# Kernel optimization log

Hardware: AMD Instinct MI355X
Metric: run time of the kernel (lower is better)

Reference implementation:

```python
import jax, jax.numpy as jnp
import numpy as np

N = 50000      # n_nodes
E = 400000     # edges per snapshot
T = 7          # end_day - start_day + 1
S = T + 1      # snapshots needed (incl. adjs[end_day+1])
NHID = 128     # nhid_gcn
NOUT = 64      # gcn output / gru input
NGRU = 64      # gru hidden
NHN = 64       # nhid_nodes
BN_EPS = 1e-5


def _unif(k, shape, fan):
    s = 1.0 / np.sqrt(fan)
    return jax.random.uniform(k, shape, jnp.float32, -s, s)


def setup_inputs() -> dict:
    key = jax.random.key(0)
    ks = jax.random.split(key, 16)
    adj_idx = jax.random.randint(ks[0], (S, 2, E), 0, N, dtype=jnp.int32)
    adj_val = jax.random.uniform(ks[1], (S, E), dtype=jnp.float32)
    return {
        'adj_idx': adj_idx, 'adj_val': adj_val,
        'start_day': 0, 'end_day': 6,
        # GCN layers (uniform(-1/sqrt(out), 1/sqrt(out)) like reset_parameters)
        'W1': _unif(ks[2], (N, NHID), NHID), 'b1': _unif(ks[3], (NHID,), NHID),
        'W2': _unif(ks[4], (NHID, NOUT), NOUT), 'b2': _unif(ks[5], (NOUT,), NOUT),
        # GRU (torch layout: [3*H, in] / [3*H, H], gate order r,z,n)
        'w_ih': _unif(ks[6], (3 * NGRU, NOUT), NGRU), 'w_hh': _unif(ks[7], (3 * NGRU, NGRU), NGRU),
        'b_ih': _unif(ks[8], (3 * NGRU,), NGRU), 'b_hh': _unif(ks[9], (3 * NGRU,), NGRU),
        'bn_gamma': jnp.ones((NGRU,), jnp.float32), 'bn_beta': jnp.zeros((NGRU,), jnp.float32),
        'attn_w': _unif(ks[10], (2 * NGRU, 1), 2 * NGRU), 'attn_b': _unif(ks[11], (1,), 2 * NGRU),
        'np_w1': _unif(ks[12], (2 * NGRU, NHN), 2 * NGRU), 'np_b1': _unif(ks[13], (NHN,), 2 * NGRU),
        'np_w2': _unif(ks[14], (NHN, 2), NHN), 'np_b2': _unif(ks[15], (2,), NHN),
    }


def _spmm(row, col, val, x):
    # sparse.mm(adj, x): out[r] = sum_{(r,c)} val * x[c]
    return jax.ops.segment_sum(val[:, None] * x[col], row, num_segments=N)


def _forward(adj_idx, start_day, end_day, adj_val, W1, b1, W2, b2,
             w_ih, w_hh, b_ih, b_hh, bn_gamma, bn_beta,
             attn_w, attn_b, np_w1, np_b1, np_w2, np_b2):
    seq_idx = adj_idx[start_day:end_day + 1]   # [T,2,E]
    seq_val = adj_val[start_day:end_day + 1]   # [T,E]

    def step(h, ts):
        idx, val = ts
        row, col = idx[0], idx[1]
        # GCN layer 1: feat is identity => support == W1
        x = jax.nn.relu(_spmm(row, col, val, W1) + b1)           # [N,NHID]
        # GCN layer 2 (no activation on last layer)
        x = _spmm(row, col, val, x @ W2) + b2                    # [N,NOUT]
        # GRU cell (batch = nodes)
        gi = x @ w_ih.T + b_ih
        gh = h @ w_hh.T + b_hh
        ir, iz, in_ = jnp.split(gi, 3, axis=1)
        hr, hz, hn = jnp.split(gh, 3, axis=1)
        r = jax.nn.sigmoid(ir + hr)
        z = jax.nn.sigmoid(iz + hz)
        n = jnp.tanh(in_ + r * hn)
        return (1.0 - z) * n + z * h, None

    h0 = jnp.zeros((N, NGRU), adj_val.dtype)
    final_emb, _ = jax.lax.scan(step, h0, (seq_idx, seq_val))    # [N,NGRU]

    # BatchNorm1d (training-mode batch stats, biased variance)
    mean = final_emb.mean(axis=0)
    var = final_emb.var(axis=0)
    final_emb = (final_emb - mean) / jnp.sqrt(var + BN_EPS) * bn_gamma + bn_beta

    # get_node_an_scores on adjs[end_day+1]
    idx = adj_idx[end_day + 1]
    row, col = idx[0], idx[1]
    mask = row != col                                            # drop self loops
    deg = jax.ops.segment_sum(mask.astype(final_emb.dtype), row, num_segments=N)
    inv_deg = jnp.where(deg != 0, 1.0 / jnp.maximum(deg, 1.0), 1.0)
    nbr = final_emb[col]                                         # [E,NGRU]
    weights = jax.nn.sigmoid(
        jnp.concatenate([final_emb[row], nbr], axis=1) @ attn_w + attn_b)  # [E,1]
    ev = jnp.where(mask, inv_deg[row] * weights[:, 0], 0.0)
    neigh = jax.ops.segment_sum(ev[:, None] * nbr, row, num_segments=N)    # [N,NGRU]
    z = jnp.concatenate([final_emb, neigh], axis=1)
    h1 = jax.nn.relu(z @ np_w1 + np_b1)
    pred = jax.nn.log_softmax(h1 @ np_w2 + np_b2, axis=1)        # [N,2]
    return pred


def reference(adj_idx, adj_val, start_day, end_day, W1, b1, W2, b2,
              w_ih, w_hh, b_ih, b_hh, bn_gamma, bn_beta,
              attn_w, attn_b, np_w1, np_b1, np_w2, np_b2):
    return _forward(adj_idx, start_day, end_day, adj_val, W1, b1, W2, b2,
                    w_ih, w_hh, b_ih, b_hh, bn_gamma, bn_beta,
                    attn_w, attn_b, np_w1, np_b1, np_w2, np_b2)
```

## Files before the change

### kernel.cpp

```cpp
#include <hip/hip_runtime.h>
#include <math.h>

#define N_NODES 50000
#define N_EDGES 400000
#define NHID 128
#define NOUT 64
#define NGRU 64
#define BN_EPS 1e-5f
#define T_STEPS 7
#define FINAL_DAY 7
#define NPAD 50176
#define NBLK 196

__device__ __forceinline__ float sigmoidf_(float x) { return 1.f / (1.f + expf(-x)); }

__global__ void hist_kernel(const int* __restrict__ row, int* __restrict__ cnt) {
    int e = blockIdx.x * blockDim.x + threadIdx.x;
    if (e < N_EDGES) atomicAdd(&cnt[row[e]], 1);
}

__global__ void scan1_kernel(const int* __restrict__ cnt, int* __restrict__ off,
                             int* __restrict__ bsum) {
    __shared__ int s[256];
    int tid = threadIdx.x;
    int gid = blockIdx.x * 256 + tid;
    int v = cnt[gid];
    s[tid] = v;
    __syncthreads();
    for (int d = 1; d < 256; d <<= 1) {
        int t = (tid >= d) ? s[tid - d] : 0;
        __syncthreads();
        s[tid] += t;
        __syncthreads();
    }
    off[gid] = s[tid];
    if (tid == 255) bsum[blockIdx.x] = s[255];
}

__global__ void scan2_kernel(int* __restrict__ bsum) {
    __shared__ int s[256];
    int tid = threadIdx.x;
    s[tid] = (tid < NBLK) ? bsum[tid] : 0;
    __syncthreads();
    for (int d = 1; d < 256; d <<= 1) {
        int t = (tid >= d) ? s[tid - d] : 0;
        __syncthreads();
        s[tid] += t;
        __syncthreads();
    }
    if (tid < NBLK) bsum[tid] = s[tid];
}

__global__ void scan3_kernel(const int* __restrict__ cnt, int* __restrict__ off,
                             const int* __restrict__ bsum, int* __restrict__ wcur) {
    int gid = blockIdx.x * 256 + threadIdx.x;
    if (gid < N_NODES) {
        int ex = off[gid] - cnt[gid] + (blockIdx.x ? bsum[blockIdx.x - 1] : 0);
        off[gid] = ex;
        wcur[gid] = ex;
    }
    if (gid == 0) off[N_NODES] = N_EDGES;
}

__global__ void scatter_kernel(const int* __restrict__ row, const int* __restrict__ col,
                               const float* __restrict__ val, int* __restrict__ wcur,
                               int* __restrict__ colp, float* __restrict__ valp) {
    int e = blockIdx.x * blockDim.x + threadIdx.x;
    if (e >= N_EDGES) return;
    int r = row[e];
    int p = atomicAdd(&wcur[r], 1);
    colp[p] = col[e];
    valp[p] = val[e];
}

__global__ __launch_bounds__(256) void fused_gcn_gather(
    const int* __restrict__ off, const int* __restrict__ colp,
    const float* __restrict__ valp, const float* __restrict__ W1,
    const float* __restrict__ b1, const float* __restrict__ W2,
    float* __restrict__ y) {
    int lane = threadIdx.x & 63;
    float wcol[NHID];
#pragma unroll
    for (int k = 0; k < NHID; ++k) wcol[k] = W2[(size_t)k * NOUT + lane];
    float b1a = b1[lane * 2], b1b = b1[lane * 2 + 1];
    int wave = (blockIdx.x * blockDim.x + threadIdx.x) >> 6;
    int nwaves = (gridDim.x * blockDim.x) >> 6;
    for (int n = wave; n < N_NODES; n += nwaves) {
        int beg = off[n], end = off[n + 1];
        float accx = 0.f, accy = 0.f;
        for (int base = beg; base < end; base += 64) {
            int m = end - base; if (m > 64) m = 64;
            int ce = 0; float ve = 0.f;
            if (lane < m) { ce = colp[base + lane]; ve = valp[base + lane]; }
#pragma unroll 4
            for (int k = 0; k < m; ++k) {
                int c = __shfl(ce, k);
                float v = __shfl(ve, k);
                const float2 w = *reinterpret_cast<const float2*>(W1 + (size_t)c * NHID + lane * 2);
                accx += v * w.x; accy += v * w.y;
            }
        }
        float xa = fmaxf(accx + b1a, 0.f);
        float xb = fmaxf(accy + b1b, 0.f);
        float acc = 0.f;
#pragma unroll
        for (int k2 = 0; k2 < 64; ++k2) {
            float x0 = __shfl(xa, k2);
            float x1v = __shfl(xb, k2);
            acc += x0 * wcol[2 * k2] + x1v * wcol[2 * k2 + 1];
        }
        y[(size_t)n * NOUT + lane] = acc;
    }
}

__global__ __launch_bounds__(256) void spmm2_gather(
    const int* __restrict__ off, const int* __restrict__ colp,
    const float* __restrict__ valp, const float* __restrict__ y,
    float* __restrict__ x2) {
    int lane = threadIdx.x & 63;
    int wave = (blockIdx.x * blockDim.x + threadIdx.x) >> 6;
    int nwaves = (gridDim.x * blockDim.x) >> 6;
    for (int n = wave; n < N_NODES; n += nwaves) {
        int beg = off[n], end = off[n + 1];
        float acc = 0.f;
        for (int base = beg; base < end; base += 64) {
            int m = end - base; if (m > 64) m = 64;
            int ce = 0; float ve = 0.f;
            if (lane < m) { ce = colp[base + lane]; ve = valp[base + lane]; }
#pragma unroll 4
            for (int k = 0; k < m; ++k) {
                int c = __shfl(ce, k);
                float v = __shfl(ve, k);
                acc += v * y[(size_t)c * NOUT + lane];
            }
        }
        x2[(size_t)n * NOUT + lane] = acc;
    }
}

__global__ void bias_fold(const float* __restrict__ w_ih, const float* __restrict__ b2,
                          const float* __restrict__ b_ih, float* __restrict__ bias_i) {
    int f = blockIdx.x * 64 + threadIdx.x;
    if (f >= 192) return;
    float acc = b_ih[f];
    for (int k = 0; k < 64; ++k) acc += w_ih[(size_t)f * 64 + k] * b2[k];
    bias_i[f] = acc;
}

__global__ __launch_bounds__(256) void gru_gemm(const float* __restrict__ x2,
                                                const float* __restrict__ w_ih,
                                                const float* __restrict__ w_hh,
                                                const float* __restrict__ bias_i,
                                                const float* __restrict__ b_hh,
                                                float* __restrict__ h) {
    __shared__ float XT[64 * 64];
    __shared__ float WT[64 * 192];
    int tid = threadIdx.x;
    int n0 = blockIdx.x * 64;
    int tf = tid & 15, tn = tid >> 4;

    float gi[4][12], gh[4][12];
#pragma unroll
    for (int i = 0; i < 4; ++i)
#pragma unroll
        for (int j = 0; j < 12; ++j) { gi[i][j] = 0.f; gh[i][j] = 0.f; }

#pragma unroll
    for (int r = 0; r < 4; ++r) {
        int idx = r * 256 + tid;
        int n = idx & 63, c4 = idx >> 6;
        int node = n0 + n;
        float4 v = make_float4(0.f, 0.f, 0.f, 0.f);
        if (node < N_NODES) v = *reinterpret_cast<const float4*>(x2 + (size_t)node * 64 + c4 * 4);
        XT[(c4 * 4 + 0) * 64 + n] = v.x;
        XT[(c4 * 4 + 1) * 64 + n] = v.y;
        XT[(c4 * 4 + 2) * 64 + n] = v.z;
        XT[(c4 * 4 + 3) * 64 + n] = v.w;
    }
#pragma unroll
    for (int r = 0; r < 12; ++r) {
        int idx = r * 256 + tid;
        int f = idx % 192, c4 = idx / 192;
        float4 v = *reinterpret_cast<const float4*>(w_ih + (size_t)f * 64 + c4 * 4);
        WT[(c4 * 4 + 0) * 192 + f] = v.x;
        WT[(c4 * 4 + 1) * 192 + f] = v.y;
        WT[(c4 * 4 + 2) * 192 + f] = v.z;
        WT[(c4 * 4 + 3) * 192 + f] = v.w;
    }
    __syncthreads();

#pragma unroll 4
    for (int k = 0; k < 64; ++k) {
        float4 a  = *reinterpret_cast<const float4*>(XT + k * 64 + tn * 4);
        float4 br = *reinterpret_cast<const float4*>(WT + k * 192 + tf * 4);
        float4 bz = *reinterpret_cast<const float4*>(WT + k * 192 + 64 + tf * 4);
        float4 bn = *reinterpret_cast<const float4*>(WT + k * 192 + 128 + tf * 4);
        float av[4] = {a.x, a.y, a.z, a.w};
#pragma unroll
        for (int i = 0; i < 4; ++i) {
            gi[i][0] += av[i] * br.x; gi[i][1] += av[i] * br.y;
            gi[i][2] += av[i] * br.z; gi[i][3] += av[i] * br.w;
            gi[i][4] += av[i] * bz.x; gi[i][5] += av[i] * bz.y;
            gi[i][6] += av[i] * bz.z; gi[i][7] += av[i] * bz.w;
            gi[i][8] += av[i] * bn.x; gi[i][9] += av[i] * bn.y;
            gi[i][10] += av[i] * bn.z; gi[i][11] += av[i] * bn.w;
        }
    }
    __syncthreads();

#pragma unroll
    for (int r = 0; r < 4; ++r) {
        int idx = r * 256 + tid;
        int n = idx & 63, c4 = idx >> 6;
        int node = n0 + n;
        float4 v = make_float4(0.f, 0.f, 0.f, 0.f);
        if (node < N_NODES) v = *reinterpret_cast<const float4*>(h + (size_t)node * 64 + c4 * 4);
        XT[(c4 * 4 + 0) * 64 + n] = v.x;
        XT[(c4 * 4 + 1) * 64 + n] = v.y;
        XT[(c4 * 4 + 2) * 64 + n] = v.z;
        XT[(c4 * 4 + 3) * 64 + n] = v.w;
    }
#pragma unroll
    for (int r = 0; r < 12; ++r) {
        int idx = r * 256 + tid;
        int f = idx % 192, c4 = idx / 192;
        float4 v = *reinterpret_cast<const float4*>(w_hh + (size_t)f * 64 + c4 * 4);
        WT[(c4 * 4 + 0) * 192 + f] = v.x;
        WT[(c4 * 4 + 1) * 192 + f] = v.y;
        WT[(c4 * 4 + 2) * 192 + f] = v.z;
        WT[(c4 * 4 + 3) * 192 + f] = v.w;
    }
    __syncthreads();

#pragma unroll 4
    for (int k = 0; k < 64; ++k) {
        float4 a  = *reinterpret_cast<const float4*>(XT + k * 64 + tn * 4);
        float4 br = *reinterpret_cast<const float4*>(WT + k * 192 + tf * 4);
        float4 bz = *reinterpret_cast<const float4*>(WT + k * 192 + 64 + tf * 4);
        float4 bn = *reinterpret_cast<const float4*>(WT + k * 192 + 128 + tf * 4);
        float av[4] = {a.x, a.y, a.z, a.w};
#pragma unroll
        for (int i = 0; i < 4; ++i) {
            gh[i][0] += av[i] * br.x; gh[i][1] += av[i] * br.y;
            gh[i][2] += av[i] * br.z; gh[i][3] += av[i] * br.w;
            gh[i][4] += av[i] * bz.x; gh[i][5] += av[i] * bz.y;
            gh[i][6] += av[i] * bz.z; gh[i][7] += av[i] * bz.w;
            gh[i][8] += av[i] * bn.x; gh[i][9] += av[i] * bn.y;
            gh[i][10] += av[i] * bn.z; gh[i][11] += av[i] * bn.w;
        }
    }

    int f0 = tf * 4;
    float bir[4], biz[4], bin_[4], bhr[4], bhz[4], bhn[4];
#pragma unroll
    for (int j = 0; j < 4; ++j) {
        bir[j] = bias_i[f0 + j];
        biz[j] = bias_i[64 + f0 + j];
        bin_[j] = bias_i[128 + f0 + j];
        bhr[j] = b_hh[f0 + j];
        bhz[j] = b_hh[64 + f0 + j];
        bhn[j] = b_hh[128 + f0 + j];
    }
#pragma unroll
    for (int i = 0; i < 4; ++i) {
        int node = n0 + tn * 4 + i;
        float hnew[4];
#pragma unroll
        for (int j = 0; j < 4; ++j) {
            float r = sigmoidf_(gi[i][j] + bir[j] + gh[i][j] + bhr[j]);
            float z = sigmoidf_(gi[i][4 + j] + biz[j] + gh[i][4 + j] + bhz[j]);
            float nn = tanhf(gi[i][8 + j] + bin_[j] + r * (gh[i][8 + j] + bhn[j]));
            float hold = XT[(f0 + j) * 64 + tn * 4 + i];
            hnew[j] = (1.f - z) * nn + z * hold;
        }
        if (node < N_NODES) {
            float4 v = make_float4(hnew[0], hnew[1], hnew[2], hnew[3]);
            *reinterpret_cast<float4*>(h + (size_t)node * 64 + f0) = v;
        }
    }
}

__global__ void bn_stats(const float* __restrict__ h, float* __restrict__ bnsum,
                         float* __restrict__ bnsq) {
    int gid = blockIdx.x * blockDim.x + threadIdx.x;
    int wave = gid >> 6, lane = gid & 63;
    int nw = (gridDim.x * blockDim.x) >> 6;
    float s = 0.f, sq = 0.f;
    for (int n = wave; n < N_NODES; n += nw) {
        float v = h[(size_t)n * NGRU + lane];
        s += v; sq += v * v;
    }
    atomicAdd(&bnsum[lane], s);
    atomicAdd(&bnsq[lane], sq);
}

__global__ void bn_norm(float* __restrict__ h, const float* __restrict__ bnsum,
                        const float* __restrict__ bnsq, const float* __restrict__ gamma,
                        const float* __restrict__ beta) {
    int gid = blockIdx.x * blockDim.x + threadIdx.x;
    if (gid >= N_NODES * NGRU) return;
    int f = gid & 63;
    float mean = bnsum[f] * (1.f / N_NODES);
    float var = bnsq[f] * (1.f / N_NODES) - mean * mean;
    float scale = gamma[f] * rsqrtf(var + BN_EPS);
    h[gid] = (h[gid] - mean) * scale + beta[f];
}

__global__ __launch_bounds__(256) void attn_gather(
    const int* __restrict__ off, const int* __restrict__ colp,
    const float* __restrict__ emb, const float* __restrict__ attn_w,
    const float* __restrict__ attn_b, float* __restrict__ neigh) {
    int lane = threadIdx.x & 63;
    float aw1 = attn_w[lane], aw2 = attn_w[64 + lane];
    float ab0 = attn_b[0];
    int wave = (blockIdx.x * blockDim.x + threadIdx.x) >> 6;
    int nwaves = (gridDim.x * blockDim.x) >> 6;
    for (int r = wave; r < N_NODES; r += nwaves) {
        float er = emb[(size_t)r * NGRU + lane];
        float pr = er * aw1;
#pragma unroll
        for (int o = 32; o > 0; o >>= 1) pr += __shfl_xor(pr, o);
        int beg = off[r], end = off[r + 1];
        float acc = 0.f;
        int cntv = 0;
        for (int base = beg; base < end; base += 64) {
            int m = end - base; if (m > 64) m = 64;
            int ce = 0;
            if (lane < m) ce = colp[base + lane];
            for (int k = 0; k < m; ++k) {
                int c = __shfl(ce, k);
                if (c == r) continue;
                float ec = emb[(size_t)c * NGRU + lane];
                float pe = ec * aw2;
#pragma unroll
                for (int o = 32; o > 0; o >>= 1) pe += __shfl_xor(pe, o);
                float wgt = sigmoidf_(pr + pe + ab0);
                acc += wgt * ec;
                ++cntv;
            }
        }
        float d = (float)cntv;
        float inv = (d != 0.f) ? 1.f / fmaxf(d, 1.f) : 1.f;
        neigh[(size_t)r * NGRU + lane] = acc * inv;
    }
}

__global__ __launch_bounds__(256) void pred_kernel(const float* __restrict__ emb,
                                                   const float* __restrict__ neigh,
                                                   const float* __restrict__ np_w1,
                                                   const float* __restrict__ np_b1,
                                                   const float* __restrict__ np_w2,
                                                   const float* __restrict__ np_b2,
                                                   float* __restrict__ out) {
    int lane = threadIdx.x & 63;
    float wcol[128];
#pragma unroll
    for (int k = 0; k < 128; ++k) wcol[k] = np_w1[(size_t)k * 64 + lane];
    float b1l = np_b1[lane];
    float w20 = np_w2[lane * 2], w21 = np_w2[lane * 2 + 1];
    float b20 = np_b2[0], b21 = np_b2[1];
    int wave = (blockIdx.x * blockDim.x + threadIdx.x) >> 6;
    int nwaves = (gridDim.x * blockDim.x) >> 6;
    for (int n = wave; n < N_NODES; n += nwaves) {
        float ev = emb[(size_t)n * 64 + lane];
        float nv = neigh[(size_t)n * 64 + lane];
        float acc = b1l;
#pragma unroll
        for (int k2 = 0; k2 < 64; ++k2) {
            float e = __shfl(ev, k2);
            float nn = __shfl(nv, k2);
            acc += e * wcol[k2] + nn * wcol[64 + k2];
        }
        float h1 = fmaxf(acc, 0.f);
        float l0 = h1 * w20, l1 = h1 * w21;
#pragma unroll
        for (int o = 32; o > 0; o >>= 1) {
            l0 += __shfl_xor(l0, o);
            l1 += __shfl_xor(l1, o);
        }
        if (lane == 0) {
            l0 += b20; l1 += b21;
            float m = fmaxf(l0, l1);
            float ls = m + logf(expf(l0 - m) + expf(l1 - m));
            out[(size_t)n * 2 + 0] = l0 - ls;
            out[(size_t)n * 2 + 1] = l1 - ls;
        }
    }
}

extern "C" void kernel_launch(void* const* d_in, const int* in_sizes, int n_in,
                              void* d_out, int out_size, void* d_ws, size_t ws_size,
                              hipStream_t stream) {
    const int* adj_idx = (const int*)d_in[0];
    const float* adj_val = (const float*)d_in[1];
    const float* W1 = (const float*)d_in[4];
    const float* b1 = (const float*)d_in[5];
    const float* W2 = (const float*)d_in[6];
    const float* b2 = (const float*)d_in[7];
    const float* w_ih = (const float*)d_in[8];
    const float* w_hh = (const float*)d_in[9];
    const float* b_ih = (const float*)d_in[10];
    const float* b_hh = (const float*)d_in[11];
    const float* bn_gamma = (const float*)d_in[12];
    const float* bn_beta = (const float*)d_in[13];
    const float* attn_w = (const float*)d_in[14];
    const float* attn_b = (const float*)d_in[15];
    const float* np_w1 = (const float*)d_in[16];
    const float* np_b1 = (const float*)d_in[17];
    const float* np_w2 = (const float*)d_in[18];
    const float* np_b2 = (const float*)d_in[19];
    float* out = (float*)d_out;

    float* ws = (float*)d_ws;
    float* y = ws;
    float* x2 = ws + (size_t)N_NODES * 64;
    float* h = ws + (size_t)N_NODES * 128;
    size_t p = (size_t)N_NODES * 192;
    int* off = (int*)(ws + p);    p += NPAD + 1;
    int* wcur = (int*)(ws + p);   p += N_NODES;
    int* cnt = (int*)(ws + p);    p += NPAD;
    int* bsum = (int*)(ws + p);   p += 256;
    int* colp = (int*)(ws + p);   p += N_EDGES;
    float* valp = ws + p;         p += N_EDGES;
    float* bnsum = ws + p;        p += 64;
    float* bnsq = ws + p;         p += 64;
    float* bias_i = ws + p;       p += 192;
    float* neigh = y;

    hipMemsetAsync(h, 0, (size_t)N_NODES * 64 * sizeof(float), stream);
    bias_fold<<<3, 64, 0, stream>>>(w_ih, b2, b_ih, bias_i);

    const int egrid = (N_EDGES + 255) / 256;
    const int gtiles = (N_NODES + 63) / 64;

    for (int t = 0; t < T_STEPS; ++t) {
        const int* row = adj_idx + (size_t)t * 2 * N_EDGES;
        const int* colr = row + N_EDGES;
        const float* val = adj_val + (size_t)t * N_EDGES;
        hipMemsetAsync(cnt, 0, NPAD * sizeof(int), stream);
        hist_kernel<<<egrid, 256, 0, stream>>>(row, cnt);
        scan1_kernel<<<NBLK, 256, 0, stream>>>(cnt, off, bsum);
        scan2_kernel<<<1, 256, 0, stream>>>(bsum);
        scan3_kernel<<<NBLK, 256, 0, stream>>>(cnt, off, bsum, wcur);
        scatter_kernel<<<egrid, 256, 0, stream>>>(row, colr, val, wcur, colp, valp);
        fused_gcn_gather<<<512, 256, 0, stream>>>(off, colp, valp, W1, b1, W2, y);
        spmm2_gather<<<512, 256, 0, stream>>>(off, colp, valp, y, x2);
        gru_gemm<<<gtiles, 256, 0, stream>>>(x2, w_ih, w_hh, bias_i, b_hh, h);
    }

    hipMemsetAsync(bnsum, 0, 2 * 64 * sizeof(float), stream);
    bn_stats<<<256, 256, 0, stream>>>(h, bnsum, bnsq);
    bn_norm<<<(N_NODES * 64 + 255) / 256, 256, 0, stream>>>(h, bnsum, bnsq, bn_gamma, bn_beta);

    const int* row7 = adj_idx + (size_t)FINAL_DAY * 2 * N_EDGES;
    const int* col7 = row7 + N_EDGES;
    hipMemsetAsync(cnt, 0, NPAD * sizeof(int), stream);
    hist_kernel<<<egrid, 256, 0, stream>>>(row7, cnt);
    scan1_kernel<<<NBLK, 256, 0, stream>>>(cnt, off, bsum);
    scan2_kernel<<<1, 256, 0, stream>>>(bsum);
    scan3_kernel<<<NBLK, 256, 0, stream>>>(cnt, off, bsum, wcur);
    scatter_kernel<<<egrid, 256, 0, stream>>>(row7, col7, adj_val + (size_t)FINAL_DAY * N_EDGES, wcur, colp, valp);
    attn_gather<<<512, 256, 0, stream>>>(off, colp, h, attn_w, attn_b, neigh);
    pred_kernel<<<512, 256, 0, stream>>>(h, neigh, np_w1, np_b1, np_w2, np_b2, out);
}
```

Measured before the change: 2.699 ms.

## Batch CSR builds across days, stage W2 in LDS, precompute attention projections

Builds the row histograms and prefix-scan offsets for all eight snapshots in one set of batched launches instead of five launches per day. This cuts launch count and serialization. The GCN kernel now keeps W2 in shared memory instead of 128 per-lane registers, which should relieve register pressure and raise occupancy at the cost of LDS reads in the inner loop. The attention stage precomputes the per-node neighbor projection once and computes the sigmoid weights per edge in parallel, replacing a 64-lane reduction for every edge.

```diff
diff --git a/kernel.cpp b/kernel.cpp
--- a/kernel.cpp
+++ b/kernel.cpp
@@ -9,22 +9,28 @@
 #define BN_EPS 1e-5f
 #define T_STEPS 7
 #define FINAL_DAY 7
+#define NDAYS 8
 #define NPAD 50176
 #define NBLK 196
+#define OFFS (NPAD + 1)
 
 __device__ __forceinline__ float sigmoidf_(float x) { return 1.f / (1.f + expf(-x)); }
 
-__global__ void hist_kernel(const int* __restrict__ row, int* __restrict__ cnt) {
-    int e = blockIdx.x * blockDim.x + threadIdx.x;
-    if (e < N_EDGES) atomicAdd(&cnt[row[e]], 1);
-}
-
-__global__ void scan1_kernel(const int* __restrict__ cnt, int* __restrict__ off,
-                             int* __restrict__ bsum) {
+__global__ void hist8_kernel(const int* __restrict__ adj_idx, int* __restrict__ cnt8) {
+    int g = blockIdx.x * blockDim.x + threadIdx.x;
+    if (g >= NDAYS * N_EDGES) return;
+    int day = g / N_EDGES, idx = g - day * N_EDGES;
+    int r = adj_idx[(size_t)day * 2 * N_EDGES + idx];
+    atomicAdd(&cnt8[day * NPAD + r], 1);
+}
+
+__global__ void scan1_8(const int* __restrict__ cnt8, int* __restrict__ off8,
+                        int* __restrict__ bsum8) {
     __shared__ int s[256];
+    int day = blockIdx.x / NBLK, blk = blockIdx.x - day * NBLK;
     int tid = threadIdx.x;
-    int gid = blockIdx.x * 256 + tid;
-    int v = cnt[gid];
+    int gid = blk * 256 + tid;
+    int v = cnt8[day * NPAD + gid];
     s[tid] = v;
     __syncthreads();
     for (int d = 1; d < 256; d <<= 1) {
@@ -33,14 +39,15 @@
         s[tid] += t;
         __syncthreads();
     }
-    off[gid] = s[tid];
-    if (tid == 255) bsum[blockIdx.x] = s[255];
-}
-
-__global__ void scan2_kernel(int* __restrict__ bsum) {
+    off8[day * OFFS + gid] = s[tid];
+    if (tid == 255) bsum8[day * NBLK + blk] = s[255];
+}
+
+__global__ void scan2_8(int* __restrict__ bsum8) {
     __shared__ int s[256];
+    int day = blockIdx.x;
     int tid = threadIdx.x;
-    s[tid] = (tid < NBLK) ? bsum[tid] : 0;
+    s[tid] = (tid < NBLK) ? bsum8[day * NBLK + tid] : 0;
     __syncthreads();
     for (int d = 1; d < 256; d <<= 1) {
         int t = (tid >= d) ? s[tid - d] : 0;
@@ -48,18 +55,20 @@
         s[tid] += t;
         __syncthreads();
     }
-    if (tid < NBLK) bsum[tid] = s[tid];
-}
-
-__global__ void scan3_kernel(const int* __restrict__ cnt, int* __restrict__ off,
-                             const int* __restrict__ bsum, int* __restrict__ wcur) {
-    int gid = blockIdx.x * 256 + threadIdx.x;
+    if (tid < NBLK) bsum8[day * NBLK + tid] = s[tid];
+}
+
+__global__ void scan3_8(const int* __restrict__ cnt8, int* __restrict__ off8,
+                        const int* __restrict__ bsum8, int* __restrict__ wcur8) {
+    int day = blockIdx.x / NBLK, blk = blockIdx.x - day * NBLK;
+    int gid = blk * 256 + threadIdx.x;
     if (gid < N_NODES) {
-        int ex = off[gid] - cnt[gid] + (blockIdx.x ? bsum[blockIdx.x - 1] : 0);
-        off[gid] = ex;
-        wcur[gid] = ex;
-    }
-    if (gid == 0) off[N_NODES] = N_EDGES;
+        int ex = off8[day * OFFS + gid] - cnt8[day * NPAD + gid]
+               + (blk ? bsum8[day * NBLK + blk - 1] : 0);
+        off8[day * OFFS + gid] = ex;
+        wcur8[day * N_NODES + gid] = ex;
+    }
+    if (gid == 0) off8[day * OFFS + N_NODES] = N_EDGES;
 }
 
 __global__ void scatter_kernel(const int* __restrict__ row, const int* __restrict__ col,
@@ -78,10 +87,14 @@
     const float* __restrict__ valp, const float* __restrict__ W1,
     const float* __restrict__ b1, const float* __restrict__ W2,
     float* __restrict__ y) {
+    __shared__ float W2s[NHID * NOUT];
+    {
+        const float4* src = reinterpret_cast<const float4*>(W2);
+        float4* dst = reinterpret_cast<float4*>(W2s);
+        for (int i = threadIdx.x; i < NHID * NOUT / 4; i += 256) dst[i] = src[i];
+    }
+    __syncthreads();
     int lane = threadIdx.x & 63;
-    float wcol[NHID];
-#pragma unroll
-    for (int k = 0; k < NHID; ++k) wcol[k] = W2[(size_t)k * NOUT + lane];
     float b1a = b1[lane * 2], b1b = b1[lane * 2 + 1];
     int wave = (blockIdx.x * blockDim.x + threadIdx.x) >> 6;
     int nwaves = (gridDim.x * blockDim.x) >> 6;
@@ -107,7 +120,7 @@
         for (int k2 = 0; k2 < 64; ++k2) {
             float x0 = __shfl(xa, k2);
             float x1v = __shfl(xb, k2);
-            acc += x0 * wcol[2 * k2] + x1v * wcol[2 * k2 + 1];
+            acc += x0 * W2s[(2 * k2) * 64 + lane] + x1v * W2s[(2 * k2 + 1) * 64 + lane];
         }
         y[(size_t)n * NOUT + lane] = acc;
     }
@@ -306,12 +319,28 @@
     h[gid] = (h[gid] - mean) * scale + beta[f];
 }
 
+__global__ __launch_bounds__(256) void attn_pre(const float* __restrict__ emb,
+                                                const float* __restrict__ attn_w,
+                                                float* __restrict__ pe) {
+    int lane = threadIdx.x & 63;
+    float aw2 = attn_w[64 + lane];
+    int wave = (blockIdx.x * blockDim.x + threadIdx.x) >> 6;
+    int nwaves = (gridDim.x * blockDim.x) >> 6;
+    for (int n = wave; n < N_NODES; n += nwaves) {
+        float p = emb[(size_t)n * NGRU + lane] * aw2;
+#pragma unroll
+        for (int o = 32; o > 0; o >>= 1) p += __shfl_xor(p, o);
+        if (lane == 0) pe[n] = p;
+    }
+}
+
 __global__ __launch_bounds__(256) void attn_gather(
     const int* __restrict__ off, const int* __restrict__ colp,
     const float* __restrict__ emb, const float* __restrict__ attn_w,
-    const float* __restrict__ attn_b, float* __restrict__ neigh) {
+    const float* __restrict__ attn_b, const float* __restrict__ pe,
+    float* __restrict__ neigh) {
     int lane = threadIdx.x & 63;
-    float aw1 = attn_w[lane], aw2 = attn_w[64 + lane];
+    float aw1 = attn_w[lane];
     float ab0 = attn_b[0];
     int wave = (blockIdx.x * blockDim.x + threadIdx.x) >> 6;
     int nwaves = (gridDim.x * blockDim.x) >> 6;
@@ -322,25 +351,24 @@
         for (int o = 32; o > 0; o >>= 1) pr += __shfl_xor(pr, o);
         int beg = off[r], end = off[r + 1];
         float acc = 0.f;
-        int cntv = 0;
+        float fcnt = 0.f;
         for (int base = beg; base < end; base += 64) {
             int m = end - base; if (m > 64) m = 64;
-            int ce = 0;
-            if (lane < m) ce = colp[base + lane];
+            int ce = 0; float pc = 0.f;
+            if (lane < m) { ce = colp[base + lane]; pc = pe[ce]; }
+            bool valid = (lane < m) && (ce != r);
+            float wl = valid ? sigmoidf_(pr + pc + ab0) : 0.f;
+            fcnt += valid ? 1.f : 0.f;
             for (int k = 0; k < m; ++k) {
                 int c = __shfl(ce, k);
                 if (c == r) continue;
-                float ec = emb[(size_t)c * NGRU + lane];
-                float pe = ec * aw2;
-#pragma unroll
-                for (int o = 32; o > 0; o >>= 1) pe += __shfl_xor(pe, o);
-                float wgt = sigmoidf_(pr + pe + ab0);
-                acc += wgt * ec;
-                ++cntv;
+                float w = __shfl(wl, k);
+                acc += w * emb[(size_t)c * NGRU + lane];
             }
         }
-        float d = (float)cntv;
-        float inv = (d != 0.f) ? 1.f / fmaxf(d, 1.f) : 1.f;
+#pragma unroll
+        for (int o = 32; o > 0; o >>= 1) fcnt += __shfl_xor(fcnt, o);
+        float inv = (fcnt != 0.f) ? 1.f / fmaxf(fcnt, 1.f) : 1.f;
         neigh[(size_t)r * NGRU + lane] = acc * inv;
     }
 }
@@ -416,19 +444,26 @@
     float* x2 = ws + (size_t)N_NODES * 64;
     float* h = ws + (size_t)N_NODES * 128;
     size_t p = (size_t)N_NODES * 192;
-    int* off = (int*)(ws + p);    p += NPAD + 1;
-    int* wcur = (int*)(ws + p);   p += N_NODES;
-    int* cnt = (int*)(ws + p);    p += NPAD;
-    int* bsum = (int*)(ws + p);   p += 256;
+    int* off8 = (int*)(ws + p);   p += (size_t)NDAYS * OFFS;
+    int* wcur8 = (int*)(ws + p);  p += (size_t)NDAYS * N_NODES;
+    int* cnt8 = (int*)(ws + p);   p += (size_t)NDAYS * NPAD;
+    int* bsum8 = (int*)(ws + p);  p += 2048;
     int* colp = (int*)(ws + p);   p += N_EDGES;
     float* valp = ws + p;         p += N_EDGES;
     float* bnsum = ws + p;        p += 64;
     float* bnsq = ws + p;         p += 64;
     float* bias_i = ws + p;       p += 192;
+    float* pe = ws + p;           p += N_NODES;
     float* neigh = y;
 
     hipMemsetAsync(h, 0, (size_t)N_NODES * 64 * sizeof(float), stream);
+    hipMemsetAsync(cnt8, 0, (size_t)NDAYS * NPAD * sizeof(int), stream);
     bias_fold<<<3, 64, 0, stream>>>(w_ih, b2, b_ih, bias_i);
+
+    hist8_kernel<<<(NDAYS * N_EDGES + 255) / 256, 256, 0, stream>>>(adj_idx, cnt8);
+    scan1_8<<<NDAYS * NBLK, 256, 0, stream>>>(cnt8, off8, bsum8);
+    scan2_8<<<NDAYS, 256, 0, stream>>>(bsum8);
+    scan3_8<<<NDAYS * NBLK, 256, 0, stream>>>(cnt8, off8, bsum8, wcur8);
 
     const int egrid = (N_EDGES + 255) / 256;
     const int gtiles = (N_NODES + 63) / 64;
@@ -437,12 +472,8 @@
         const int* row = adj_idx + (size_t)t * 2 * N_EDGES;
         const int* colr = row + N_EDGES;
         const float* val = adj_val + (size_t)t * N_EDGES;
-        hipMemsetAsync(cnt, 0, NPAD * sizeof(int), stream);
-        hist_kernel<<<egrid, 256, 0, stream>>>(row, cnt);
-        scan1_kernel<<<NBLK, 256, 0, stream>>>(cnt, off, bsum);
-        scan2_kernel<<<1, 256, 0, stream>>>(bsum);
-        scan3_kernel<<<NBLK, 256, 0, stream>>>(cnt, off, bsum, wcur);
-        scatter_kernel<<<egrid, 256, 0, stream>>>(row, colr, val, wcur, colp, valp);
+        const int* off = off8 + (size_t)t * OFFS;
+        scatter_kernel<<<egrid, 256, 0, stream>>>(row, colr, val, wcur8 + (size_t)t * N_NODES, colp, valp);
         fused_gcn_gather<<<512, 256, 0, stream>>>(off, colp, valp, W1, b1, W2, y);
         spmm2_gather<<<512, 256, 0, stream>>>(off, colp, valp, y, x2);
         gru_gemm<<<gtiles, 256, 0, stream>>>(x2, w_ih, w_hh, bias_i, b_hh, h);
@@ -454,12 +485,10 @@
 
     const int* row7 = adj_idx + (size_t)FINAL_DAY * 2 * N_EDGES;
     const int* col7 = row7 + N_EDGES;
-    hipMemsetAsync(cnt, 0, NPAD * sizeof(int), stream);
-    hist_kernel<<<egrid, 256, 0, stream>>>(row7, cnt);
-    scan1_kernel<<<NBLK, 256, 0, stream>>>(cnt, off, bsum);
-    scan2_kernel<<<1, 256, 0, stream>>>(bsum);
-    scan3_kernel<<<NBLK, 256, 0, stream>>>(cnt, off, bsum, wcur);
-    scatter_kernel<<<egrid, 256, 0, stream>>>(row7, col7, adj_val + (size_t)FINAL_DAY * N_EDGES, wcur, colp, valp);
-    attn_gather<<<512, 256, 0, stream>>>(off, colp, h, attn_w, attn_b, neigh);
+    const int* off7 = off8 + (size_t)FINAL_DAY * OFFS;
+    scatter_kernel<<<egrid, 256, 0, stream>>>(row7, col7, adj_val + (size_t)FINAL_DAY * N_EDGES,
+                                              wcur8 + (size_t)FINAL_DAY * N_NODES, colp, valp);
+    attn_pre<<<256, 256, 0, stream>>>(h, attn_w, pe);
+    attn_gather<<<512, 256, 0, stream>>>(off7, colp, h, attn_w, attn_b, pe, neigh);
     pred_kernel<<<512, 256, 0, stream>>>(h, neigh, np_w1, np_b1, np_w2, np_b2, out);
 }
```

After: 2.573 ms. 4.7% less time.
